# Kernel tuning notes

Measured on AMD Instinct MI355X. Metric: run time of the kernel, lower is better.

Reference implementation:

```python
import jax, jax.numpy as jnp
import numpy as np

B, N, E = 64, 2048, 32768          # graphs, nodes/graph, edges/graph
DIM = 64
RATIO = 0.8
K1 = int(np.ceil(RATIO * N))        # 1639 nodes/graph after pool1
K2 = int(np.ceil(RATIO * K1))       # 1312 nodes/graph after pool2
NUM_CLASSES = 6


def gcn_conv(x, W, b, src, dst, valid, n):
    # GCNConv with self-loops: out = D^-1/2 (A+I) D^-1/2 (x W) + b
    xw = x @ W                                          # [n, DIM]
    deg = jnp.zeros(n, x.dtype).at[dst].add(valid) + 1.0  # in-degree incl. self-loop
    norm = valid * jax.lax.rsqrt(deg[src] * deg[dst])      # per-edge norm (0 for masked)
    agg = jnp.zeros_like(xw).at[dst].add(xw[src] * norm[:, None])
    return agg + xw / deg[:, None] + b                  # self-loop term has norm 1/deg


def topk_pool(x, p, n_graphs, n_per, k):
    # PyG TopKPooling: score = tanh(x.p/||p||); keep top-k per graph; gate x by score
    score = jnp.tanh((x @ p) / jnp.linalg.norm(p))       # [n_graphs*n_per]
    vals, idx = jax.lax.top_k(score.reshape(n_graphs, n_per), k)  # [n_graphs, k]
    xg = x.reshape(n_graphs, n_per, -1)
    sel = jnp.take_along_axis(xg, idx[..., None], axis=1)          # [n_graphs, k, DIM]
    xp = sel * vals[..., None]
    perm = (idx + (jnp.arange(n_graphs) * n_per)[:, None]).reshape(-1)  # global ids kept
    return xp.reshape(n_graphs * k, -1), perm


def global_max_mean(x, n_graphs, n_per):
    xg = x.reshape(n_graphs, n_per, -1)
    return jnp.concatenate([xg.max(axis=1), xg.mean(axis=1)], axis=1)  # [n_graphs, 2*DIM]


def forward(x, edge_index, batch, W1, b1, p1, W2, b2, p2, lin1_w, lin1_b, lin2_w, lin2_b):
    src, dst = edge_index[0], edge_index[1]
    n_total = B * N
    ones = jnp.ones(src.shape[0], x.dtype)

    x = jax.nn.relu(gcn_conv(x, W1, b1, src, dst, ones, n_total))
    x, perm = topk_pool(x, p1, B, N, K1)
    x1 = global_max_mean(x, B, K1)

    # filter_adj: reindex edges to surviving nodes; drop (mask) edges touching removed nodes
    new_id = jnp.full(n_total, -1, jnp.int32).at[perm].set(jnp.arange(B * K1, dtype=jnp.int32))
    s2, d2 = new_id[src], new_id[dst]
    valid = ((s2 >= 0) & (d2 >= 0)).astype(x.dtype)
    s2 = jnp.where(s2 >= 0, s2, 0)
    d2 = jnp.where(d2 >= 0, d2, 0)

    x = jax.nn.relu(gcn_conv(x, W2, b2, s2, d2, valid, B * K1))
    x, _ = topk_pool(x, p2, B, K1, K2)
    x2 = global_max_mean(x, B, K2)

    h = x1 + x2
    h = jax.nn.relu(h @ lin1_w + lin1_b)
    return h @ lin2_w + lin2_b                           # [B, NUM_CLASSES]


def setup_inputs():
    key = jax.random.key(0)
    ks = jax.random.split(key, 10)
    x = jax.random.normal(ks[0], (B * N, DIM), jnp.float32)
    off = (jnp.arange(B) * N)[:, None]
    src = (jax.random.randint(ks[1], (B, E), 0, N) + off).reshape(-1)
    dst = (jax.random.randint(ks[2], (B, E), 0, N) + off).reshape(-1)
    edge_index = jnp.stack([src, dst]).astype(jnp.int32)
    batch = jnp.repeat(jnp.arange(B, dtype=jnp.int32), N)
    s = 1.0 / np.sqrt(DIM)
    return {
        "x": x,
        "edge_index": edge_index,
        "batch": batch,
        "W1": jax.random.normal(ks[3], (DIM, DIM), jnp.float32) * s,
        "b1": jnp.zeros(DIM, jnp.float32),
        "p1": jax.random.normal(ks[4], (DIM,), jnp.float32) * s,
        "W2": jax.random.normal(ks[5], (DIM, DIM), jnp.float32) * s,
        "b2": jnp.zeros(DIM, jnp.float32),
        "p2": jax.random.normal(ks[6], (DIM,), jnp.float32) * s,
        "lin1_w": jax.random.normal(ks[7], (2 * DIM, DIM), jnp.float32) / np.sqrt(2 * DIM),
        "lin1_b": jnp.zeros(DIM, jnp.float32),
        "lin2_w": jax.random.normal(ks[8], (DIM, NUM_CLASSES), jnp.float32) * s,
        "lin2_b": jnp.zeros(NUM_CLASSES, jnp.float32),
    }


def reference(x, edge_index, batch, W1, b1, p1, W2, b2, p2, lin1_w, lin1_b, lin2_w, lin2_b):
    return forward(x, edge_index, batch, W1, b1, p1, W2, b2, p2, lin1_w, lin1_b, lin2_w, lin2_b)
```

## Files before the change

### kernel.cpp

```cpp
#include <hip/hip_runtime.h>
#include <hip/hip_bf16.h>
#include <cstdint>
#include <cstddef>

#define B_    64
#define N_    2048
#define E_    32768
#define DIM_  64
#define K1_   1639
#define K2_   1312
#define NTOT  (B_ * N_)
#define ETOT  (B_ * E_)
#define N2TOT (B_ * K1_)
#define NCLS  6
#define PB_   8
#define CHUNKS_ 16
#define SLICES_ 16
#define BCAP  3072
#define REG_  192

typedef short bf8 __attribute__((ext_vector_type(8)));
typedef float f4  __attribute__((ext_vector_type(4)));

static __device__ __forceinline__ float2 bf2f(unsigned u) {
    float2 r;
    r.x = __uint_as_float(u << 16);
    r.y = __uint_as_float(u & 0xFFFF0000u);
    return r;
}
static __device__ __forceinline__ unsigned f2bf(float a, float b) {
    __hip_bfloat162 h = __float22bfloat162_rn(make_float2(a, b));
    unsigned u;
    __builtin_memcpy(&u, &h, 4);
    return u;
}
static __device__ __forceinline__ unsigned short f2bf_rn(float v) {
    unsigned u = __float_as_uint(v);
    return (unsigned short)((u + 0x7FFFu + ((u >> 16) & 1u)) >> 16);
}
static __device__ __forceinline__ unsigned long long mk_key(float s, int i) {
    unsigned u = __float_as_uint(s);
    u = (u & 0x80000000u) ? ~u : (u | 0x80000000u);
    return ((unsigned long long)u << 11) | (unsigned long long)(2047 - i);
}

template<int STAGE>
__launch_bounds__(256)
__global__ void k_bucket(const int* src, const int* dst, const int* remap,
                         int* bcnt, unsigned int* blist) {
    const int LSTR = (STAGE == 1) ? 128 : 103;
    __shared__ unsigned int lb[CHUNKS_][REG_];
    __shared__ int lc[CHUNKS_];
    __shared__ int rm[N_];
    int b = blockIdx.x;
    int g = b & 63, slice = b >> 6;
    int tid = threadIdx.x;
    if (tid < CHUNKS_) lc[tid] = 0;
    if (STAGE == 2)
        for (int i = tid; i < N_; i += 256) rm[i] = remap[g * N_ + i];
    __syncthreads();
    const int ESL = E_ / SLICES_;
    const int* sp = src + (size_t)g * E_ + slice * ESL;
    const int* dp = dst + (size_t)g * E_ + slice * ESL;
    int gbase = g * ((STAGE == 1) ? N_ : K1_);
    for (int e = tid * 4; e < ESL; e += 1024) {
        int4 ss = *(const int4*)&sp[e];
        int4 dd = *(const int4*)&dp[e];
#pragma unroll
        for (int t = 0; t < 4; t++) {
            int s = (&ss.x)[t], d = (&dd.x)[t];
            if (STAGE == 2) {
                s = rm[s & (N_ - 1)]; d = rm[d & (N_ - 1)];
                if ((s | d) < 0) continue;
                s -= gbase; d -= gbase;
            } else {
                s &= (N_ - 1); d &= (N_ - 1);
            }
            int ch = d / LSTR;
            int dl = d - ch * LSTR;
            int p = atomicAdd(&lc[ch], 1);
            if (p < REG_) lb[ch][p] = ((unsigned)dl << 12) | (unsigned)s;
        }
    }
    __syncthreads();
    for (int ch = 0; ch < CHUNKS_; ch++) {
        int n = min(lc[ch], REG_);
        unsigned int* out = blist + (size_t)(g * CHUNKS_ + ch) * BCAP + slice * REG_;
        for (int i = tid; i < n; i += 256) out[i] = lb[ch][i];
    }
    if (tid < CHUNKS_) bcnt[(g * SLICES_ + slice) * CHUNKS_ + tid] = min(lc[tid], REG_);
}

template<int STAGE>
__launch_bounds__(256)
__global__ void k_sort(const int* bcnt, unsigned int* blist,
                       const float* xf, const unsigned int* xg,
                       unsigned int* xb, int* ninfo) {
    const int NL   = (STAGE == 1) ? N_ : K1_;
    const int LSTR = (STAGE == 1) ? 128 : 103;
    __shared__ int cnt[128], st[128], cur[128], cnt_s[SLICES_], stot[2];
    __shared__ float rsqv[128];
    __shared__ unsigned short sorted[BCAP];
    int b = blockIdx.x;
    int g = b & 63, ch = b >> 6;
    int tid = threadIdx.x;
    if (tid < 128) { cnt[tid] = 0; cur[tid] = 0; }
    if (tid < SLICES_) cnt_s[tid] = bcnt[(g * SLICES_ + tid) * CHUNKS_ + ch];
    __syncthreads();
    size_t bb = (size_t)(g * CHUNKS_ + ch) * BCAP;
    const unsigned int* bl = blist + bb;
    const int TOT = SLICES_ * REG_;
    for (int i = tid; i < TOT; i += 256) {
        int s = i / REG_, j = i - s * REG_;
        if (j < cnt_s[s]) atomicAdd(&cnt[bl[i] >> 12], 1);
    }
    __syncthreads();
    if (tid < 128) {
        int v = cnt[tid];
        int l64 = tid & 63;
#pragma unroll
        for (int o = 1; o < 64; o <<= 1) {
            int t = __shfl_up(v, o);
            if (l64 >= o) v += t;
        }
        st[tid] = v;
        if (l64 == 63) stot[tid >> 6] = v;
    }
    __syncthreads();
    if (tid >= 64 && tid < 128) st[tid] += stot[0];
    __syncthreads();
    for (int i = tid; i < TOT; i += 256) {
        int s = i / REG_, j = i - s * REG_;
        if (j < cnt_s[s]) {
            unsigned pk = bl[i];
            int dl = (int)(pk >> 12);
            int p = st[dl] - cnt[dl] + atomicAdd(&cur[dl], 1);
            sorted[p] = (unsigned short)(pk & 0xFFFu);
        }
    }
    __syncthreads();
    int n = st[127];
    for (int i = tid; i < n; i += 256) blist[bb + i] = ((unsigned int)sorted[i]) << 5;
    int lo = ch * LSTR;
    int nloc = min(LSTR, NL - lo);
    int gbase = g * NL;
    if (tid < nloc) {
        int node = gbase + lo + tid;
        int c = cnt[tid];
        int start = (int)bb + st[tid] - c;
        ninfo[node] = (start << 8) | min(c, 255);
        rsqv[tid] = rsqrtf((float)(c + 1));
    }
    __syncthreads();
    for (int idx = tid; idx < nloc * 32; idx += 256) {
        int nl = idx >> 5, f2 = idx & 31;
        int node = gbase + lo + nl;
        float sc = rsqv[nl];
        float2 v;
        if (STAGE == 1) v = ((const float2*)xf)[(size_t)node * 32 + f2];
        else            v = bf2f(xg[(size_t)node * 32 + f2]);
        xb[(size_t)node * 32 + f2] = f2bf(v.x * sc, v.y * sc);
    }
}

template<bool GATE>
__launch_bounds__(256)
__global__ void k_aggconv(const unsigned int* xb, const int* ninfo, const unsigned int* csr,
                          const float* W, const float* bias, const float* pvec,
                          float* y, float* score) {
    const int NL = GATE ? K1_ : N_;
    __shared__ float4 ls4[1024];
    float* ls = (float*)ls4;
    int b = blockIdx.x;
    int wg;
    if (GATE) {
        int xcd = b & 7, k = b >> 3;
        wg = (xcd < 7 ? xcd * 205 : 1435 + (xcd - 7) * 204) + k;
    } else {
        wg = (b & 7) * 256 + (b >> 3);
    }
    int wid = threadIdx.x >> 6, lane = threadIdx.x & 63;
    int half = lane >> 5;
    int l32 = lane & 31;
    int hbase = half << 5;
    int rowbase = wg * 64 + wid * 16;

    int niv = 0;
    if (lane < 16) niv = ninfo[rowbase + lane];
    int ni = __shfl(niv, half);
    int sv = 0;
    {
        int c0 = ni & 255;
        if (l32 < c0) sv = (int)csr[(ni >> 8) + l32];
    }
#pragma unroll 1
    for (int p = 0; p < 8; p++) {
        int cnt = ni & 255, base = ni >> 8;
        int ni_n = 0, sv_n = 0;
        if (p < 7) {
            ni_n = __shfl(niv, 2 * (p + 1) + half);
            int cn = ni_n & 255;
            if (l32 < cn) sv_n = (int)csr[(ni_n >> 8) + l32];
        }
        int rloc = wid * 16 + 2 * p + half;
        int node = wg * 64 + rloc;
        int gbase32 = GATE ? (node / K1_) * (K1_ * 32) : ((node & ~(N_ - 1)) * 32);
        unsigned selfu = xb[(size_t)node * 32 + l32];
        float a0x = 0.f, a0y = 0.f, a1x = 0.f, a1y = 0.f;
        float a2x = 0.f, a2y = 0.f, a3x = 0.f, a3y = 0.f;
        int svc = sv;
        for (int chunk = 0; chunk < cnt; chunk += 32) {
            int nch = min(32, cnt - chunk);
            if (chunk) svc = (l32 < nch) ? (int)csr[base + chunk + l32] : 0;
            int i = 0;
            for (; i + 8 <= nch; i += 8) {
                int e0 = __shfl(svc, hbase + i);
                int e1 = __shfl(svc, hbase + i + 1);
                int e2 = __shfl(svc, hbase + i + 2);
                int e3 = __shfl(svc, hbase + i + 3);
                int e4 = __shfl(svc, hbase + i + 4);
                int e5 = __shfl(svc, hbase + i + 5);
                int e6 = __shfl(svc, hbase + i + 6);
                int e7 = __shfl(svc, hbase + i + 7);
                unsigned u0 = xb[(size_t)(gbase32 + e0 + l32)];
                unsigned u1 = xb[(size_t)(gbase32 + e1 + l32)];
                unsigned u2 = xb[(size_t)(gbase32 + e2 + l32)];
                unsigned u3 = xb[(size_t)(gbase32 + e3 + l32)];
                unsigned u4 = xb[(size_t)(gbase32 + e4 + l32)];
                unsigned u5 = xb[(size_t)(gbase32 + e5 + l32)];
                unsigned u6 = xb[(size_t)(gbase32 + e6 + l32)];
                unsigned u7 = xb[(size_t)(gbase32 + e7 + l32)];
                float2 f0 = bf2f(u0), f1 = bf2f(u1), f2 = bf2f(u2), f3 = bf2f(u3);
                float2 f4 = bf2f(u4), f5 = bf2f(u5), f6 = bf2f(u6), f7 = bf2f(u7);
                a0x += f0.x; a0y += f0.y;
                a1x += f1.x; a1y += f1.y;
                a2x += f2.x; a2y += f2.y;
                a3x += f3.x; a3y += f3.y;
                a0x += f4.x; a0y += f4.y;
                a1x += f5.x; a1y += f5.y;
                a2x += f6.x; a2y += f6.y;
                a3x += f7.x; a3y += f7.y;
            }
            for (; i + 4 <= nch; i += 4) {
                int e0 = __shfl(svc, hbase + i);
                int e1 = __shfl(svc, hbase + i + 1);
                int e2 = __shfl(svc, hbase + i + 2);
                int e3 = __shfl(svc, hbase + i + 3);
                unsigned u0 = xb[(size_t)(gbase32 + e0 + l32)];
                unsigned u1 = xb[(size_t)(gbase32 + e1 + l32)];
                unsigned u2 = xb[(size_t)(gbase32 + e2 + l32)];
                unsigned u3 = xb[(size_t)(gbase32 + e3 + l32)];
                float2 f0 = bf2f(u0), f1 = bf2f(u1), f2 = bf2f(u2), f3 = bf2f(u3);
                a0x += f0.x; a0y += f0.y;
                a1x += f1.x; a1y += f1.y;
                a2x += f2.x; a2y += f2.y;
                a3x += f3.x; a3y += f3.y;
            }
            for (; i < nch; i++) {
                int e0 = __shfl(svc, hbase + i);
                float2 f0 = bf2f(xb[(size_t)(gbase32 + e0 + l32)]);
                a0x += f0.x; a0y += f0.y;
            }
        }
        float rd = rsqrtf((float)(cnt + 1));
        float sx = (a0x + a1x) + (a2x + a3x);
        float sy = (a0y + a1y) + (a2y + a3y);
        float2 fs = bf2f(selfu);
        float2 o;
        o.x = (sx + fs.x) * rd;
        o.y = (sy + fs.y) * rd;
        int pi = rloc * 32 + ((((l32 >> 1) ^ (rloc & 7)) << 1) | (l32 & 1));
        ((float2*)ls)[pi] = o;
        ni = ni_n; sv = sv_n;
    }
    __syncthreads();

    int q = lane >> 4, c = lane & 15;
    bf8 bh[2][4], blo[2][4];
#pragma unroll
    for (int ks = 0; ks < 2; ks++)
#pragma unroll
        for (int nt = 0; nt < 4; nt++) {
            bf8 h, l;
#pragma unroll
            for (int j = 0; j < 8; j++) {
                float wv = W[(ks * 32 + q * 8 + j) * 64 + nt * 16 + c];
                unsigned short hb = f2bf_rn(wv);
                h[j] = (short)hb;
                l[j] = (short)f2bf_rn(wv - __uint_as_float((unsigned)hb << 16));
            }
            bh[ks][nt] = h; blo[ks][nt] = l;
        }
    int rl16 = (wid * 16 + c) * 16;
    int cx = c & 7;
    bf8 ah[2], al[2];
#pragma unroll
    for (int ks = 0; ks < 2; ks++) {
        float4 v0 = ls4[rl16 + ((ks * 8 + q * 2 + 0) ^ cx)];
        float4 v1 = ls4[rl16 + ((ks * 8 + q * 2 + 1) ^ cx)];
        float vv[8] = {v0.x, v0.y, v0.z, v0.w, v1.x, v1.y, v1.z, v1.w};
        bf8 h, l;
#pragma unroll
        for (int j = 0; j < 8; j++) {
            unsigned short hb = f2bf_rn(vv[j]);
            h[j] = (short)hb;
            l[j] = (short)f2bf_rn(vv[j] - __uint_as_float((unsigned)hb << 16));
        }
        ah[ks] = h; al[ks] = l;
    }
    float pp = 0.f;
#pragma unroll
    for (int i = 0; i < DIM_; i++) pp += pvec[i] * pvec[i];
    float rpn = rsqrtf(pp);
    float dot[4] = {0.f, 0.f, 0.f, 0.f};
#pragma unroll
    for (int nt = 0; nt < 4; nt++) {
        f4 acc = {0.f, 0.f, 0.f, 0.f};
#pragma unroll
        for (int ks = 0; ks < 2; ks++) {
            acc = __builtin_amdgcn_mfma_f32_16x16x32_bf16(ah[ks], bh[ks][nt],  acc, 0, 0, 0);
            acc = __builtin_amdgcn_mfma_f32_16x16x32_bf16(ah[ks], blo[ks][nt], acc, 0, 0, 0);
            acc = __builtin_amdgcn_mfma_f32_16x16x32_bf16(al[ks], bh[ks][nt],  acc, 0, 0, 0);
        }
        float bcol = bias[nt * 16 + c];
        float pcol = pvec[nt * 16 + c];
        float st[4];
#pragma unroll
        for (int reg = 0; reg < 4; reg++) {
            float v = fmaxf(acc[reg] + bcol, 0.f);
            st[reg] = v;
            dot[reg] += v * pcol;
        }
#pragma unroll
        for (int reg = 0; reg < 4; reg++)
            y[(size_t)(wg * 64 + wid * 16 + q * 4 + reg) * DIM_ + nt * 16 + c] = st[reg];
    }
#pragma unroll
    for (int m = 1; m < 16; m <<= 1) {
#pragma unroll
        for (int reg = 0; reg < 4; reg++) dot[reg] += __shfl_xor(dot[reg], m);
    }
    if (c == 0) {
#pragma unroll
        for (int reg = 0; reg < 4; reg++)
            score[wg * 64 + wid * 16 + q * 4 + reg] = tanhf(dot[reg] * rpn);
    }
}

template<int STAGE>
__launch_bounds__(256)
__global__ void k_thresh(const float* score, unsigned long long* thresh) {
    const int Nin = (STAGE == 1) ? N_ : K1_;
    const int K   = (STAGE == 1) ? K1_ : K2_;
    __shared__ unsigned long long keys[N_];
    __shared__ int bins[256], wsum[4];
    __shared__ unsigned long long s_prefix;
    __shared__ int s_need;
    int g = blockIdx.x, tid = threadIdx.x;
    int l64 = tid & 63, wid = tid >> 6;
    const float* sg = score + (size_t)g * Nin;
    for (int i = tid; i < Nin; i += 256) keys[i] = mk_key(sg[i], i);
    if (tid == 0) { s_need = K; s_prefix = 0ull; }
    __syncthreads();
    for (int shift = 40; shift >= 0; shift -= 8) {
        bins[tid] = 0;
        __syncthreads();
        unsigned long long pref = s_prefix;
        int need = s_need;
        int hi = shift + 8;
        for (int i = tid; i < Nin; i += 256) {
            unsigned long long k = keys[i];
            if ((k >> hi) == pref) atomicAdd(&bins[(int)((k >> shift) & 255)], 1);
        }
        __syncthreads();
        int mine = bins[tid];
        int v = mine;
#pragma unroll
        for (int o = 1; o < 64; o <<= 1) {
            int t = __shfl_down(v, o);
            if (l64 + o < 64) v += t;
        }
        if (l64 == 0) wsum[wid] = v;
        __syncthreads();
        for (int w = wid + 1; w < 4; w++) v += wsum[w];
        int nxt = v - mine;
        if (v >= need && nxt < need) {
            s_prefix = (pref << 8) | (unsigned long long)tid;
            s_need = need - nxt;
        }
        __syncthreads();
    }
    if (tid == 0) thresh[g] = s_prefix;
}

template<int STAGE>
__launch_bounds__(256)
__global__ void k_pool(const float* score, const float* conv, const unsigned long long* thresh,
                       int* new_id, unsigned int* xg, float* part) {
    const int Nin = (STAGE == 1) ? N_ : K1_;
    const int RNG = (STAGE == 1) ? (N_ / PB_) : ((K1_ + PB_ - 1) / PB_);
    __shared__ int rnk[256];
    __shared__ unsigned char keepf[256];
    __shared__ int wsum[4], s_base[4];
    __shared__ float rmx[4][64], rsm[4][64];
    int b = blockIdx.x;
    int g = b & 63, pb = b >> 6;
    int tid = threadIdx.x;
    int l64 = tid & 63, wid = tid >> 6;
    const float* sg = score + (size_t)g * Nin;
    unsigned long long T = thresh[g];
    int R0 = pb * RNG;
    int R1 = min(R0 + RNG, Nin);
    if (STAGE == 1) {
        int cb = 0;
        for (int i = tid; i < R0; i += 256) cb += (mk_key(sg[i], i) >= T) ? 1 : 0;
#pragma unroll
        for (int o = 32; o; o >>= 1) cb += __shfl_down(cb, o);
        if (l64 == 0) s_base[wid] = cb;
        int i = R0 + tid;
        int keep = (i < R1 && mk_key(sg[i], i) >= T) ? 1 : 0;
        keepf[tid] = (unsigned char)keep;
        int v = keep;
#pragma unroll
        for (int o = 1; o < 64; o <<= 1) {
            int t = __shfl_up(v, o);
            if (l64 >= o) v += t;
        }
        if (l64 == 63) wsum[wid] = v;
        __syncthreads();
        int base = s_base[0] + s_base[1] + s_base[2] + s_base[3];
        int wbase = 0;
        for (int w = 0; w < wid; w++) wbase += wsum[w];
        int r = base + wbase + v - keep;
        rnk[tid] = r;
        if (i < Nin) new_id[g * N_ + i] = keep ? (g * K1_ + r) : -1;
    } else {
        int i = R0 + tid;
        keepf[tid] = (unsigned char)((i < R1 && mk_key(sg[i], i) >= T) ? 1 : 0);
    }
    __syncthreads();
    float mx = -3.402823466e38f, sm = 0.f;
    for (int i = R0 + wid; i < R1; i += 4) {
        if (!keepf[i - R0]) continue;
        float val = sg[i];
        float v = conv[(size_t)(g * Nin + i) * DIM_ + l64] * val;
        mx = fmaxf(mx, v);
        sm += v;
        if (STAGE == 1) {
            unsigned pk = f2bf(v, __shfl_xor(v, 1));
            if (!(l64 & 1)) xg[(size_t)(g * K1_ + rnk[i - R0]) * 32 + (l64 >> 1)] = pk;
        }
    }
    rmx[wid][l64] = mx; rsm[wid][l64] = sm;
    __syncthreads();
    if (wid == 0) {
        mx = fmaxf(fmaxf(rmx[0][l64], rmx[1][l64]), fmaxf(rmx[2][l64], rmx[3][l64]));
        sm = rsm[0][l64] + rsm[1][l64] + rsm[2][l64] + rsm[3][l64];
        part[((size_t)(g * PB_ + pb) * 2 + 0) * 64 + l64] = mx;
        part[((size_t)(g * PB_ + pb) * 2 + 1) * 64 + l64] = sm;
    }
}

__launch_bounds__(64)
__global__ void k_head(const float* part1, const float* part2,
                       const float* l1w, const float* l1b,
                       const float* l2w, const float* l2b, float* out) {
    __shared__ float h[128];
    __shared__ float h1[64];
    int g = blockIdx.x, t = threadIdx.x;
    float mx1 = -3.402823466e38f, sm1 = 0.f, mx2 = -3.402823466e38f, sm2 = 0.f;
#pragma unroll
    for (int c = 0; c < PB_; c++) {
        mx1 = fmaxf(mx1, part1[((size_t)(g * PB_ + c) * 2 + 0) * 64 + t]);
        sm1 += part1[((size_t)(g * PB_ + c) * 2 + 1) * 64 + t];
        mx2 = fmaxf(mx2, part2[((size_t)(g * PB_ + c) * 2 + 0) * 64 + t]);
        sm2 += part2[((size_t)(g * PB_ + c) * 2 + 1) * 64 + t];
    }
    h[t]      = mx1 + mx2;
    h[t + 64] = sm1 / (float)K1_ + sm2 / (float)K2_;
    __syncthreads();
    float acc = l1b[t];
#pragma unroll 8
    for (int i = 0; i < 128; i++) acc += h[i] * l1w[i * 64 + t];
    h1[t] = fmaxf(acc, 0.0f);
    __syncthreads();
    if (t < NCLS) {
        float o = l2b[t];
#pragma unroll
        for (int i = 0; i < 64; i++) o += h1[i] * l2w[i * NCLS + t];
        out[g * NCLS + t] = o;
    }
}

extern "C" void kernel_launch(void* const* d_in, const int* in_sizes, int n_in,
                              void* d_out, int out_size, void* d_ws, size_t ws_size,
                              hipStream_t stream) {
    const float* x   = (const float*)d_in[0];
    const int*   ei  = (const int*)d_in[1];
    const int*   src = ei;
    const int*   dst = ei + ETOT;
    const float* W1  = (const float*)d_in[3];
    const float* b1  = (const float*)d_in[4];
    const float* p1  = (const float*)d_in[5];
    const float* W2  = (const float*)d_in[6];
    const float* b2  = (const float*)d_in[7];
    const float* p2  = (const float*)d_in[8];
    const float* l1w = (const float*)d_in[9];
    const float* l1b = (const float*)d_in[10];
    const float* l2w = (const float*)d_in[11];
    const float* l2b = (const float*)d_in[12];
    (void)in_sizes; (void)n_in; (void)out_size; (void)ws_size;

    char* ws = (char*)d_ws;
    size_t off = 0;
    auto alloc = [&](size_t bytes) -> void* {
        void* p = ws + off;
        off = (off + bytes + 255) & ~(size_t)255;
        return p;
    };
    float*              bufA   = (float*)             alloc((size_t)NTOT  * DIM_ * 4);
    float*              bufB   = (float*)             alloc((size_t)N2TOT * DIM_ * 4);
    unsigned int*       blist  = (unsigned int*)      alloc((size_t)B_ * CHUNKS_ * BCAP * 4);
    unsigned int*       xb     = (unsigned int*)      alloc((size_t)NTOT * 32 * 4);
    int*                bcnt   = (int*)               alloc((size_t)B_ * SLICES_ * CHUNKS_ * 4);
    int*                ninfo  = (int*)               alloc((size_t)NTOT * 4);
    float*              score  = (float*)             alloc((size_t)NTOT * 4);
    int*                newid  = (int*)               alloc((size_t)NTOT * 4);
    unsigned long long* thr    = (unsigned long long*)alloc((size_t)B_ * 8);
    float*              part1  = (float*)             alloc((size_t)B_ * PB_ * 128 * 4);
    float*              part2  = (float*)             alloc((size_t)B_ * PB_ * 128 * 4);
    unsigned int*       xg     = (unsigned int*)bufB;

    k_bucket<1><<<B_ * SLICES_, 256, 0, stream>>>(src, dst, nullptr, bcnt, blist);
    k_sort<1><<<B_ * CHUNKS_, 256, 0, stream>>>(bcnt, blist, x, nullptr, xb, ninfo);
    k_aggconv<false><<<NTOT / 64, 256, 0, stream>>>(xb, ninfo, blist, W1, b1, p1, bufA, score);
    k_thresh<1><<<B_, 256, 0, stream>>>(score, thr);
    k_pool<1><<<B_ * PB_, 256, 0, stream>>>(score, bufA, thr, newid, xg, part1);

    k_bucket<2><<<B_ * SLICES_, 256, 0, stream>>>(src, dst, newid, bcnt, blist);
    k_sort<2><<<B_ * CHUNKS_, 256, 0, stream>>>(bcnt, blist, nullptr, xg, xb, ninfo);
    k_aggconv<true><<<N2TOT / 64, 256, 0, stream>>>(xb, ninfo, blist, W2, b2, p2, bufB, score);
    k_thresh<2><<<B_, 256, 0, stream>>>(score, thr);
    k_pool<2><<<B_ * PB_, 256, 0, stream>>>(score, bufB, thr, nullptr, nullptr, part2);

    k_head<<<B_, 64, 0, stream>>>(part1, part2, l1w, l1b, l2w, l2b, (float*)d_out);
}
```

Baseline: 321.0 us.

## Switch gather features to fp16 with fdot2 accumulation and precomputed weight fragments

Converts the staged node features from bf16 to fp16 and accumulates neighbor sums with v_dot2 instructions. The gather loop is widened to 16 loads in flight, and byte offsets are precomputed in the CSR list. The per-block split of W into bf16 hi/lo fragments is moved into a one-time k_wprep kernel, with the fragments loaded into LDS. The MFMA now uses the f16 variant with round-toward-zero packing. fp16 has a narrower range than bf16, which could overflow or lose accuracy for large activations, and the change adds one small kernel launch.

```diff
diff --git a/kernel.cpp b/kernel.cpp
--- a/kernel.cpp
+++ b/kernel.cpp
@@ -19,29 +19,43 @@
 #define BCAP  3072
 #define REG_  192
 
-typedef short bf8 __attribute__((ext_vector_type(8)));
-typedef float f4  __attribute__((ext_vector_type(4)));
-
-static __device__ __forceinline__ float2 bf2f(unsigned u) {
-    float2 r;
-    r.x = __uint_as_float(u << 16);
-    r.y = __uint_as_float(u & 0xFFFF0000u);
-    return r;
-}
-static __device__ __forceinline__ unsigned f2bf(float a, float b) {
-    __hip_bfloat162 h = __float22bfloat162_rn(make_float2(a, b));
-    unsigned u;
-    __builtin_memcpy(&u, &h, 4);
-    return u;
-}
-static __device__ __forceinline__ unsigned short f2bf_rn(float v) {
-    unsigned u = __float_as_uint(v);
-    return (unsigned short)((u + 0x7FFFu + ((u >> 16) & 1u)) >> 16);
+typedef float f4 __attribute__((ext_vector_type(4)));
+typedef _Float16 h2 __attribute__((ext_vector_type(2)));
+typedef _Float16 h8 __attribute__((ext_vector_type(8)));
+
+static __device__ __forceinline__ float fdot2(h2 a, h2 b, float c) {
+    return __builtin_amdgcn_fdot2(a, b, c, false);
+}
+static __device__ __forceinline__ h2 pkrtz(float a, float b) {
+    return __builtin_bit_cast(h2, __builtin_amdgcn_cvt_pkrtz(a, b));
 }
 static __device__ __forceinline__ unsigned long long mk_key(float s, int i) {
     unsigned u = __float_as_uint(s);
     u = (u & 0x80000000u) ? ~u : (u | 0x80000000u);
     return ((unsigned long long)u << 11) | (unsigned long long)(2047 - i);
+}
+
+__launch_bounds__(128)
+__global__ void k_wprep(const float* W1, const float* W2, h8* wf) {
+    int t = threadIdx.x;
+    int stage = t >> 6, lane = t & 63;
+    const float* W = stage ? W2 : W1;
+    int q = lane >> 4, c = lane & 15;
+#pragma unroll
+    for (int ks = 0; ks < 2; ks++)
+#pragma unroll
+        for (int nt = 0; nt < 4; nt++) {
+            h8 h, l;
+#pragma unroll
+            for (int j = 0; j < 8; j++) {
+                float wv = W[(ks * 32 + q * 8 + j) * 64 + nt * 16 + c];
+                _Float16 hh = (_Float16)wv;
+                h[j] = hh;
+                l[j] = (_Float16)(wv - (float)hh);
+            }
+            wf[(size_t)stage * 1024 + (((ks * 4 + nt) * 2 + 0) * 64) + lane] = h;
+            wf[(size_t)stage * 1024 + (((ks * 4 + nt) * 2 + 1) * 64) + lane] = l;
+        }
 }
 
 template<int STAGE>
@@ -140,7 +154,7 @@
     }
     __syncthreads();
     int n = st[127];
-    for (int i = tid; i < n; i += 256) blist[bb + i] = ((unsigned int)sorted[i]) << 5;
+    for (int i = tid; i < n; i += 256) blist[bb + i] = ((unsigned int)sorted[i]) << 7;
     int lo = ch * LSTR;
     int nloc = min(LSTR, NL - lo);
     int gbase = g * NL;
@@ -157,19 +171,24 @@
         int node = gbase + lo + nl;
         float sc = rsqv[nl];
         float2 v;
-        if (STAGE == 1) v = ((const float2*)xf)[(size_t)node * 32 + f2];
-        else            v = bf2f(xg[(size_t)node * 32 + f2]);
-        xb[(size_t)node * 32 + f2] = f2bf(v.x * sc, v.y * sc);
+        if (STAGE == 1) {
+            v = ((const float2*)xf)[(size_t)node * 32 + f2];
+        } else {
+            h2 hv = __builtin_bit_cast(h2, xg[(size_t)node * 32 + f2]);
+            v.x = (float)hv.x; v.y = (float)hv.y;
+        }
+        h2 o = {(_Float16)(v.x * sc), (_Float16)(v.y * sc)};
+        xb[(size_t)node * 32 + f2] = __builtin_bit_cast(unsigned int, o);
     }
 }
 
 template<bool GATE>
 __launch_bounds__(256)
 __global__ void k_aggconv(const unsigned int* xb, const int* ninfo, const unsigned int* csr,
-                          const float* W, const float* bias, const float* pvec,
+                          const h8* wfrag, const float* bias, const float* pvec,
                           float* y, float* score) {
-    const int NL = GATE ? K1_ : N_;
     __shared__ float4 ls4[1024];
+    __shared__ h8 wlds[2][4][2][64];
     float* ls = (float*)ls4;
     int b = blockIdx.x;
     int wg;
@@ -179,132 +198,136 @@
     } else {
         wg = (b & 7) * 256 + (b >> 3);
     }
-    int wid = threadIdx.x >> 6, lane = threadIdx.x & 63;
-    int half = lane >> 5;
-    int l32 = lane & 31;
-    int hbase = half << 5;
+    int tid = threadIdx.x;
+    int wid = tid >> 6, lane = tid & 63;
+    int half = lane >> 5, l32 = lane & 31, hbase = half << 5;
+    int l32_4 = l32 << 2;
     int rowbase = wg * 64 + wid * 16;
+
+    {
+        const h8* wsrc = wfrag + (GATE ? 1024 : 0);
+        h8* wd = (h8*)wlds;
+        for (int i = tid; i < 1024; i += 256) wd[i] = wsrc[i];
+    }
+
+    const char* xbb = (const char*)xb;
+    const h2 one0  = {(_Float16)1.0f, (_Float16)0.0f};
+    const h2 zero1 = {(_Float16)0.0f, (_Float16)1.0f};
+    int g0 = 0, bnd = 0;
+    if (GATE) { g0 = (wg * 64) / K1_; bnd = (g0 + 1) * K1_; }
+    auto gbyte = [&](int node) -> int {
+        if (GATE) { int gr = (node >= bnd) ? (g0 + 1) : g0; return gr * (K1_ * 128); }
+        return (node & ~(N_ - 1)) << 7;
+    };
 
     int niv = 0;
     if (lane < 16) niv = ninfo[rowbase + lane];
     int ni = __shfl(niv, half);
+    int gbb = gbyte(rowbase + half);
     int sv = 0;
-    {
-        int c0 = ni & 255;
-        if (l32 < c0) sv = (int)csr[(ni >> 8) + l32];
-    }
+    { int c0 = ni & 255; if (l32 < c0) sv = (int)csr[(ni >> 8) + l32] + gbb; }
 #pragma unroll 1
     for (int p = 0; p < 8; p++) {
         int cnt = ni & 255, base = ni >> 8;
-        int ni_n = 0, sv_n = 0;
+        int ni_n = 0, sv_n = 0, gbb_n = 0;
         if (p < 7) {
             ni_n = __shfl(niv, 2 * (p + 1) + half);
+            gbb_n = gbyte(rowbase + 2 * (p + 1) + half);
             int cn = ni_n & 255;
-            if (l32 < cn) sv_n = (int)csr[(ni_n >> 8) + l32];
+            if (l32 < cn) sv_n = (int)csr[(ni_n >> 8) + l32] + gbb_n;
         }
         int rloc = wid * 16 + 2 * p + half;
         int node = wg * 64 + rloc;
-        int gbase32 = GATE ? (node / K1_) * (K1_ * 32) : ((node & ~(N_ - 1)) * 32);
-        unsigned selfu = xb[(size_t)node * 32 + l32];
-        float a0x = 0.f, a0y = 0.f, a1x = 0.f, a1y = 0.f;
-        float a2x = 0.f, a2y = 0.f, a3x = 0.f, a3y = 0.f;
+        unsigned selfu = *(const unsigned*)(xbb + (unsigned)(node * 128 + l32_4));
+        float acx[4] = {0.f, 0.f, 0.f, 0.f};
+        float acy[4] = {0.f, 0.f, 0.f, 0.f};
         int svc = sv;
         for (int chunk = 0; chunk < cnt; chunk += 32) {
             int nch = min(32, cnt - chunk);
-            if (chunk) svc = (l32 < nch) ? (int)csr[base + chunk + l32] : 0;
+            if (chunk) svc = (l32 < nch) ? (int)csr[base + chunk + l32] + gbb : 0;
             int i = 0;
+            for (; i + 16 <= nch; i += 16) {
+                unsigned u[16];
+#pragma unroll
+                for (int k = 0; k < 16; k++) {
+                    int e = __shfl(svc, hbase + i + k);
+                    u[k] = *(const unsigned*)(xbb + (unsigned)(e + l32_4));
+                }
+#pragma unroll
+                for (int k = 0; k < 16; k++) {
+                    h2 h = __builtin_bit_cast(h2, u[k]);
+                    acx[k & 3] = fdot2(h, one0,  acx[k & 3]);
+                    acy[k & 3] = fdot2(h, zero1, acy[k & 3]);
+                }
+            }
             for (; i + 8 <= nch; i += 8) {
-                int e0 = __shfl(svc, hbase + i);
-                int e1 = __shfl(svc, hbase + i + 1);
-                int e2 = __shfl(svc, hbase + i + 2);
-                int e3 = __shfl(svc, hbase + i + 3);
-                int e4 = __shfl(svc, hbase + i + 4);
-                int e5 = __shfl(svc, hbase + i + 5);
-                int e6 = __shfl(svc, hbase + i + 6);
-                int e7 = __shfl(svc, hbase + i + 7);
-                unsigned u0 = xb[(size_t)(gbase32 + e0 + l32)];
-                unsigned u1 = xb[(size_t)(gbase32 + e1 + l32)];
-                unsigned u2 = xb[(size_t)(gbase32 + e2 + l32)];
-                unsigned u3 = xb[(size_t)(gbase32 + e3 + l32)];
-                unsigned u4 = xb[(size_t)(gbase32 + e4 + l32)];
-                unsigned u5 = xb[(size_t)(gbase32 + e5 + l32)];
-                unsigned u6 = xb[(size_t)(gbase32 + e6 + l32)];
-                unsigned u7 = xb[(size_t)(gbase32 + e7 + l32)];
-                float2 f0 = bf2f(u0), f1 = bf2f(u1), f2 = bf2f(u2), f3 = bf2f(u3);
-                float2 f4 = bf2f(u4), f5 = bf2f(u5), f6 = bf2f(u6), f7 = bf2f(u7);
-                a0x += f0.x; a0y += f0.y;
-                a1x += f1.x; a1y += f1.y;
-                a2x += f2.x; a2y += f2.y;
-                a3x += f3.x; a3y += f3.y;
-                a0x += f4.x; a0y += f4.y;
-                a1x += f5.x; a1y += f5.y;
-                a2x += f6.x; a2y += f6.y;
-                a3x += f7.x; a3y += f7.y;
+                unsigned u[8];
+#pragma unroll
+                for (int k = 0; k < 8; k++) {
+                    int e = __shfl(svc, hbase + i + k);
+                    u[k] = *(const unsigned*)(xbb + (unsigned)(e + l32_4));
+                }
+#pragma unroll
+                for (int k = 0; k < 8; k++) {
+                    h2 h = __builtin_bit_cast(h2, u[k]);
+                    acx[k & 3] = fdot2(h, one0,  acx[k & 3]);
+                    acy[k & 3] = fdot2(h, zero1, acy[k & 3]);
+                }
             }
             for (; i + 4 <= nch; i += 4) {
-                int e0 = __shfl(svc, hbase + i);
-                int e1 = __shfl(svc, hbase + i + 1);
-                int e2 = __shfl(svc, hbase + i + 2);
-                int e3 = __shfl(svc, hbase + i + 3);
-                unsigned u0 = xb[(size_t)(gbase32 + e0 + l32)];
-                unsigned u1 = xb[(size_t)(gbase32 + e1 + l32)];
-                unsigned u2 = xb[(size_t)(gbase32 + e2 + l32)];
-                unsigned u3 = xb[(size_t)(gbase32 + e3 + l32)];
-                float2 f0 = bf2f(u0), f1 = bf2f(u1), f2 = bf2f(u2), f3 = bf2f(u3);
-                a0x += f0.x; a0y += f0.y;
-                a1x += f1.x; a1y += f1.y;
-                a2x += f2.x; a2y += f2.y;
-                a3x += f3.x; a3y += f3.y;
+                unsigned u[4];
+#pragma unroll
+                for (int k = 0; k < 4; k++) {
+                    int e = __shfl(svc, hbase + i + k);
+                    u[k] = *(const unsigned*)(xbb + (unsigned)(e + l32_4));
+                }
+#pragma unroll
+                for (int k = 0; k < 4; k++) {
+                    h2 h = __builtin_bit_cast(h2, u[k]);
+                    acx[k] = fdot2(h, one0,  acx[k]);
+                    acy[k] = fdot2(h, zero1, acy[k]);
+                }
             }
             for (; i < nch; i++) {
-                int e0 = __shfl(svc, hbase + i);
-                float2 f0 = bf2f(xb[(size_t)(gbase32 + e0 + l32)]);
-                a0x += f0.x; a0y += f0.y;
-            }
+                int e = __shfl(svc, hbase + i);
+                h2 h = __builtin_bit_cast(h2, *(const unsigned*)(xbb + (unsigned)(e + l32_4)));
+                acx[0] = fdot2(h, one0,  acx[0]);
+                acy[0] = fdot2(h, zero1, acy[0]);
+            }
+        }
+        {
+            h2 sh = __builtin_bit_cast(h2, selfu);
+            acx[0] = fdot2(sh, one0,  acx[0]);
+            acy[0] = fdot2(sh, zero1, acy[0]);
         }
         float rd = rsqrtf((float)(cnt + 1));
-        float sx = (a0x + a1x) + (a2x + a3x);
-        float sy = (a0y + a1y) + (a2y + a3y);
-        float2 fs = bf2f(selfu);
         float2 o;
-        o.x = (sx + fs.x) * rd;
-        o.y = (sy + fs.y) * rd;
+        o.x = ((acx[0] + acx[1]) + (acx[2] + acx[3])) * rd;
+        o.y = ((acy[0] + acy[1]) + (acy[2] + acy[3])) * rd;
         int pi = rloc * 32 + ((((l32 >> 1) ^ (rloc & 7)) << 1) | (l32 & 1));
         ((float2*)ls)[pi] = o;
-        ni = ni_n; sv = sv_n;
+        ni = ni_n; sv = sv_n; gbb = gbb_n;
     }
     __syncthreads();
 
     int q = lane >> 4, c = lane & 15;
-    bf8 bh[2][4], blo[2][4];
-#pragma unroll
-    for (int ks = 0; ks < 2; ks++)
-#pragma unroll
-        for (int nt = 0; nt < 4; nt++) {
-            bf8 h, l;
-#pragma unroll
-            for (int j = 0; j < 8; j++) {
-                float wv = W[(ks * 32 + q * 8 + j) * 64 + nt * 16 + c];
-                unsigned short hb = f2bf_rn(wv);
-                h[j] = (short)hb;
-                l[j] = (short)f2bf_rn(wv - __uint_as_float((unsigned)hb << 16));
-            }
-            bh[ks][nt] = h; blo[ks][nt] = l;
-        }
     int rl16 = (wid * 16 + c) * 16;
     int cx = c & 7;
-    bf8 ah[2], al[2];
+    h8 ah[2], al[2];
 #pragma unroll
     for (int ks = 0; ks < 2; ks++) {
         float4 v0 = ls4[rl16 + ((ks * 8 + q * 2 + 0) ^ cx)];
         float4 v1 = ls4[rl16 + ((ks * 8 + q * 2 + 1) ^ cx)];
         float vv[8] = {v0.x, v0.y, v0.z, v0.w, v1.x, v1.y, v1.z, v1.w};
-        bf8 h, l;
-#pragma unroll
-        for (int j = 0; j < 8; j++) {
-            unsigned short hb = f2bf_rn(vv[j]);
-            h[j] = (short)hb;
-            l[j] = (short)f2bf_rn(vv[j] - __uint_as_float((unsigned)hb << 16));
+        h8 h, l;
+#pragma unroll
+        for (int j = 0; j < 8; j += 2) {
+            h2 hp = pkrtz(vv[j], vv[j + 1]);
+            float r0 = vv[j]     - (float)hp.x;
+            float r1 = vv[j + 1] - (float)hp.y;
+            h2 lp = pkrtz(r0, r1);
+            h[j] = hp.x; h[j + 1] = hp.y;
+            l[j] = lp.x; l[j + 1] = lp.y;
         }
         ah[ks] = h; al[ks] = l;
     }
@@ -318,9 +341,11 @@
         f4 acc = {0.f, 0.f, 0.f, 0.f};
 #pragma unroll
         for (int ks = 0; ks < 2; ks++) {
-            acc = __builtin_amdgcn_mfma_f32_16x16x32_bf16(ah[ks], bh[ks][nt],  acc, 0, 0, 0);
-            acc = __builtin_amdgcn_mfma_f32_16x16x32_bf16(ah[ks], blo[ks][nt], acc, 0, 0, 0);
-            acc = __builtin_amdgcn_mfma_f32_16x16x32_bf16(al[ks], bh[ks][nt],  acc, 0, 0, 0);
+            h8 wh = wlds[ks][nt][0][lane];
+            h8 wl = wlds[ks][nt][1][lane];
+            acc = __builtin_amdgcn_mfma_f32_16x16x32_f16(ah[ks], wh, acc, 0, 0, 0);
+            acc = __builtin_amdgcn_mfma_f32_16x16x32_f16(ah[ks], wl, acc, 0, 0, 0);
+            acc = __builtin_amdgcn_mfma_f32_16x16x32_f16(al[ks], wh, acc, 0, 0, 0);
         }
         float bcol = bias[nt * 16 + c];
         float pcol = pvec[nt * 16 + c];
@@ -447,8 +472,12 @@
         mx = fmaxf(mx, v);
         sm += v;
         if (STAGE == 1) {
-            unsigned pk = f2bf(v, __shfl_xor(v, 1));
-            if (!(l64 & 1)) xg[(size_t)(g * K1_ + rnk[i - R0]) * 32 + (l64 >> 1)] = pk;
+            float vo = __shfl_xor(v, 1);
+            if (!(l64 & 1)) {
+                h2 pk2 = {(_Float16)v, (_Float16)vo};
+                xg[(size_t)(g * K1_ + rnk[i - R0]) * 32 + (l64 >> 1)] =
+                    __builtin_bit_cast(unsigned int, pk2);
+            }
         }
     }
     rmx[wid][l64] = mx; rsm[wid][l64] = sm;
@@ -529,17 +558,20 @@
     unsigned long long* thr    = (unsigned long long*)alloc((size_t)B_ * 8);
     float*              part1  = (float*)             alloc((size_t)B_ * PB_ * 128 * 4);
     float*              part2  = (float*)             alloc((size_t)B_ * PB_ * 128 * 4);
+    h8*                 wfrag  = (h8*)                alloc((size_t)2048 * 16);
     unsigned int*       xg     = (unsigned int*)bufB;
+
+    k_wprep<<<1, 128, 0, stream>>>(W1, W2, wfrag);
 
     k_bucket<1><<<B_ * SLICES_, 256, 0, stream>>>(src, dst, nullptr, bcnt, blist);
     k_sort<1><<<B_ * CHUNKS_, 256, 0, stream>>>(bcnt, blist, x, nullptr, xb, ninfo);
-    k_aggconv<false><<<NTOT / 64, 256, 0, stream>>>(xb, ninfo, blist, W1, b1, p1, bufA, score);
+    k_aggconv<false><<<NTOT / 64, 256, 0, stream>>>(xb, ninfo, blist, wfrag, b1, p1, bufA, score);
     k_thresh<1><<<B_, 256, 0, stream>>>(score, thr);
     k_pool<1><<<B_ * PB_, 256, 0, stream>>>(score, bufA, thr, newid, xg, part1);
 
     k_bucket<2><<<B_ * SLICES_, 256, 0, stream>>>(src, dst, newid, bcnt, blist);
     k_sort<2><<<B_ * CHUNKS_, 256, 0, stream>>>(bcnt, blist, nullptr, xg, xb, ninfo);
-    k_aggconv<true><<<N2TOT / 64, 256, 0, stream>>>(xb, ninfo, blist, W2, b2, p2, bufB, score);
+    k_aggconv<true><<<N2TOT / 64, 256, 0, stream>>>(xb, ninfo, blist, wfrag, b2, p2, bufB, score);
     k_thresh<2><<<B_, 256, 0, stream>>>(score, thr);
     k_pool<2><<<B_ * PB_, 256, 0, stream>>>(score, bufB, thr, nullptr, nullptr, part2);
 
```

Measured after the change: 320.5 us. No clear change (-0.1%).
